# Kernel tuning notes

Hardware: AMD Instinct MI355X
Metric: run time of the kernel (lower is better)

The kernel has to match this reference:

```python
import jax, jax.numpy as jnp
import numpy as np

B, T, N_EMBED, HEADSIZE = 16, 2048, 1024, 128


def setup_inputs() -> dict:
    key = jax.random.key(0)
    kx, kq, kk, kv = jax.random.split(key, 4)
    x = jax.random.normal(kx, (B, T, N_EMBED), dtype=jnp.float32)
    # nn.Linear(n_embed, headsize, bias=False): y = x @ W, W stored [n_embed, headsize]
    s = (1.0 / np.sqrt(N_EMBED)).astype(np.float32)
    Wq = jax.random.normal(kq, (N_EMBED, HEADSIZE), dtype=jnp.float32) * s
    Wk = jax.random.normal(kk, (N_EMBED, HEADSIZE), dtype=jnp.float32) * s
    Wv = jax.random.normal(kv, (N_EMBED, HEADSIZE), dtype=jnp.float32) * s
    return {"x": x, "Wq": Wq, "Wk": Wk, "Wv": Wv}


def reference(x, Wq, Wk, Wv):
    Bsz, Tlen, C = x.shape
    q = x @ Wq  # [B, T, H]
    k = x @ Wk  # [B, T, H]
    v = x @ Wv  # [B, T, H]
    scale = C ** (-0.5)  # NOTE: original scales by n_embed**-0.5, not headsize**-0.5
    wt = jnp.einsum('bqh,bkh->bqk', q, k) * scale  # [B, T, T]
    causal = jnp.tril(jnp.ones((Tlen, Tlen), dtype=bool))
    wt = jnp.where(causal, wt, -jnp.inf)
    wt = jax.nn.softmax(wt, axis=-1)
    # dropout is identity in eval mode
    out = jnp.einsum('bqk,bkh->bqh', wt, v)  # [B, T, H]
    return out
```

## Files before the change

### kernel.cpp

```cpp
#include <hip/hip_runtime.h>
#include <hip/hip_bf16.h>

#define BATCH 16
#define TLEN 2048
#define CDIM 1024
#define HDIM 128

typedef __attribute__((ext_vector_type(8))) short bf16x8;
typedef __attribute__((ext_vector_type(4))) float f32x4;
typedef __attribute__((ext_vector_type(16))) float f32x16;
typedef __attribute__((ext_vector_type(4))) unsigned short u16x4;
typedef __attribute__((ext_vector_type(8))) unsigned short u16x8;

static __device__ __forceinline__ unsigned short f2bf(float f) {
    __hip_bfloat16 h = __float2bfloat16(f);
    return *(unsigned short*)&h;
}
static __device__ __forceinline__ unsigned pkbf(float a, float b) {
    return (unsigned)f2bf(a) | ((unsigned)f2bf(b) << 16);
}
static __device__ __forceinline__ int part_offs(int qc) {
    return qc + ((qc * qc - 2 * qc + (qc & 1)) >> 2);
}

typedef const __attribute__((address_space(1))) unsigned int* gas_t;
typedef __attribute__((address_space(3))) unsigned int* las_t;
static __device__ __forceinline__ void gl_lds16(const void* g, void* l) {
    __builtin_amdgcn_global_load_lds((gas_t)g, (las_t)l, 16, 0, 0);
}

__global__ __launch_bounds__(256) void pack_w(
    const float* __restrict__ Wq, const float* __restrict__ Wk,
    const float* __restrict__ Wv, unsigned short* __restrict__ wtb)
{
    const int which = blockIdx.y;
    const float* W = (which == 0) ? Wq : (which == 1) ? Wk : Wv;
    const int n = blockIdx.x >> 2;
    const int k = (blockIdx.x & 3) * 256 + threadIdx.x;
    wtb[((size_t)which * 128 + n) * 1024 + k] = f2bf(W[(size_t)k * 128 + n]);
}

__global__ __launch_bounds__(256, 2) void qkv_fused(
    const float* __restrict__ x, const unsigned short* __restrict__ wtb,
    unsigned short* __restrict__ qb, unsigned short* __restrict__ kb,
    unsigned short* __restrict__ vtb)
{
    __shared__ unsigned short Abf[2][64 * 32];
    __shared__ unsigned short Bs[2][384 * 32];

    const int tid  = threadIdx.x;
    const int lane = tid & 63, wid = tid >> 6;
    const int c = lane & 15, g = lane >> 4;
    const int m0 = blockIdx.x * 64;

    const int arow = tid >> 2;
    const int acol = (tid & 3) * 8;
    const float* xsrc = x + (size_t)(m0 + arow) * CDIM + acol;

    const int brow = lane >> 2, bcol = (lane & 3) * 8;

    f32x4 acc[4][6];
#pragma unroll
    for (int i = 0; i < 4; ++i)
#pragma unroll
        for (int j = 0; j < 6; ++j) acc[i][j] = (f32x4){0.f, 0.f, 0.f, 0.f};

    float4 a0, a1;

#define GLA(k0_)                                                             \
    { a0 = *(const float4*)(xsrc + (k0_));                                   \
      a1 = *(const float4*)(xsrc + (k0_) + 4); }

#define CVTW(bi_)                                                            \
    { u16x8 t_;                                                              \
      t_[0]=f2bf(a0.x); t_[1]=f2bf(a0.y); t_[2]=f2bf(a0.z); t_[3]=f2bf(a0.w);\
      t_[4]=f2bf(a1.x); t_[5]=f2bf(a1.y); t_[6]=f2bf(a1.z); t_[7]=f2bf(a1.w);\
      *(u16x8*)((char*)Abf[bi_] + arow * 64 + acol * 2) = t_; }

#define STB(k0_, bi_)                                                        \
    { _Pragma("unroll")                                                      \
      for (int i_ = 0; i_ < 6; ++i_) {                                       \
          const int seg_ = wid * 6 + i_;                                     \
          const unsigned short* src_ = wtb +                                 \
              (size_t)(seg_ * 16 + brow) * 1024 + (k0_) + bcol;              \
          gl_lds16(src_, (char*)Bs[bi_] + seg_ * 1024);                      \
      } }

    GLA(0);
    STB(0, 0);
    CVTW(0);
    __syncthreads();

#pragma unroll 1
    for (int kt = 0; kt < 32; ++kt) {
        const int bi = kt & 1;
        if (kt < 31) {
            GLA((kt + 1) * 32);
            STB((kt + 1) * 32, bi ^ 1);
        }

        bf16x8 af[4], bf[6];
#pragma unroll
        for (int mf = 0; mf < 4; ++mf)
            af[mf] = *(const bf16x8*)((char*)Abf[bi] + (mf * 16 + c) * 64 + g * 16);
#pragma unroll
        for (int nf = 0; nf < 6; ++nf)
            bf[nf] = *(const bf16x8*)((char*)Bs[bi] + (wid * 96 + nf * 16 + c) * 64 + g * 16);
#pragma unroll
        for (int mf = 0; mf < 4; ++mf)
#pragma unroll
            for (int nf = 0; nf < 6; ++nf)
                acc[mf][nf] = __builtin_amdgcn_mfma_f32_16x16x32_bf16(
                    af[mf], bf[nf], acc[mf][nf], 0, 0, 0);

        if (kt < 31) CVTW(bi ^ 1);
        __syncthreads();
    }

#pragma unroll
    for (int mf = 0; mf < 4; ++mf) {
#pragma unroll
        for (int nf = 0; nf < 6; ++nf) {
            const int col0 = wid * 96 + nf * 16;
            const int nt = col0 >> 7;
            const int nc = (col0 & 127) + c;
            const int m = m0 + mf * 16 + g * 4;
            if (nt == 0) {
#pragma unroll
                for (int r = 0; r < 4; ++r)
                    qb[(size_t)(m + r) * HDIM + nc] = f2bf(acc[mf][nf][r] * 0.03125f);
            } else if (nt == 1) {
#pragma unroll
                for (int r = 0; r < 4; ++r)
                    kb[(size_t)(m + r) * HDIM + nc] = f2bf(acc[mf][nf][r]);
            } else {
                const int b = m >> 11, tl = m & (TLEN - 1);
                u16x4 o;
                o[0] = f2bf(acc[mf][nf][0]); o[1] = f2bf(acc[mf][nf][1]);
                o[2] = f2bf(acc[mf][nf][2]); o[3] = f2bf(acc[mf][nf][3]);
                *(u16x4*)(vtb + ((size_t)b * HDIM + nc) * TLEN + tl) = o;
            }
        }
    }
#undef GLA
#undef CVTW
#undef STB
}

__global__ __launch_bounds__(256, 2) void attn_partial(
    const short* __restrict__ qb, const short* __restrict__ kb,
    const short* __restrict__ vtb,
    unsigned short* __restrict__ Opart, float* __restrict__ mpart,
    float* __restrict__ lpart)
{
    const int kc = blockIdx.x;
    const int qc = blockIdx.y;
    const int b  = blockIdx.z;
    if (kc > (qc >> 1)) return;
    const int kv_base = kc * 256;
    const int qrel = qc * 128 - kv_base;
    int NT = ((qrel + 127) >> 6) + 1; if (NT > 4) NT = 4;

    __shared__ unsigned short Ks[2][64 * 128];
    __shared__ unsigned short Vs[2][128 * 64];

    const int tid  = threadIdx.x;
    const int wid  = tid >> 6;
    const int lane = tid & 63;
    const int c5 = lane & 31, hi = lane >> 5;
    const int q0w = qc * 128 + wid * 32;
    const int qg  = q0w + c5;
    const int pidx = b * 72 + part_offs(qc) + kc;

    const short* Kb  = kb  + (size_t)b * TLEN * HDIM;
    const short* Vtb = vtb + (size_t)b * HDIM * TLEN;

    bf16x8 qf[8];
#pragma unroll
    for (int ks = 0; ks < 8; ++ks)
        qf[ks] = *(const bf16x8*)(qb + ((size_t)b * TLEN + qg) * HDIM + ks * 16 + hi * 8);

    bf16x8 kst[4], vst[4];

#define GLOAD(kv0_)                                                          \
    {                                                                        \
        _Pragma("unroll")                                                    \
        for (int it = 0; it < 4; ++it) {                                     \
            const int o = tid * 16 + it * 4096;                              \
            const int kr = o >> 8, kcb = o & 0xF0;                           \
            kst[it] = *(const bf16x8*)((const char*)Kb +                     \
                        (size_t)((kv0_) + kr) * 256 + kcb);                  \
            const int vr = o >> 7, vcb = o & 0x70;                           \
            vst[it] = *(const bf16x8*)((const char*)Vtb +                    \
                        (size_t)vr * (TLEN * 2) + (size_t)(kv0_) * 2 + vcb); \
        }                                                                    \
    }
#define SSTORE(bi_)                                                          \
    {                                                                        \
        _Pragma("unroll")                                                    \
        for (int it = 0; it < 4; ++it) {                                     \
            const int o = tid * 16 + it * 4096;                              \
            const int kr = o >> 8, kcb = o & 0xF0;                           \
            *(bf16x8*)((char*)Ks[bi_] + kr * 256 + (kcb ^ ((kr & 7) << 4))) = kst[it]; \
            const int vr = o >> 7, vcb = o & 0x70;                           \
            *(bf16x8*)((char*)Vs[bi_] + vr * 128 + (vcb ^ ((vr & 7) << 4))) = vst[it]; \
        }                                                                    \
    }

    GLOAD(kv_base);
    SSTORE(0);
    __syncthreads();

    f32x16 oacc[4];
#pragma unroll
    for (int i = 0; i < 4; ++i)
#pragma unroll
        for (int r = 0; r < 16; ++r) oacc[i][r] = 0.f;
    float m_r = -1e30f;
    float l_r = 0.f;

#pragma unroll 1
    for (int t = 0; t < NT; ++t) {
        const int bi = t & 1;
        if (t + 1 < NT) GLOAD(kv_base + 64 * (t + 1));

        const int kv0 = kv_base + 64 * t;
        if (kv0 <= q0w + 31) {
            f32x16 s0, s1;
#pragma unroll
            for (int r = 0; r < 16; ++r) { s0[r] = 0.f; s1[r] = 0.f; }
            __builtin_amdgcn_s_setprio(1);
#pragma unroll
            for (int ks = 0; ks < 8; ++ks) {
                const int col = ks * 32 + hi * 16;
                const int off0 = c5 * 256 + (col ^ ((c5 & 7) << 4));
                const int off1 = (32 + c5) * 256 + (col ^ ((c5 & 7) << 4));
                bf16x8 a0 = *(const bf16x8*)((char*)Ks[bi] + off0);
                bf16x8 a1 = *(const bf16x8*)((char*)Ks[bi] + off1);
                s0 = __builtin_amdgcn_mfma_f32_32x32x16_bf16(a0, qf[ks], s0, 0, 0, 0);
                s1 = __builtin_amdgcn_mfma_f32_32x32x16_bf16(a1, qf[ks], s1, 0, 0, 0);
            }
            __builtin_amdgcn_s_setprio(0);

            if (kv0 + 63 > q0w) {
#pragma unroll
                for (int r = 0; r < 16; ++r) {
                    const int key0 = kv0 + (r & 3) + 8 * (r >> 2) + 4 * hi;
                    if (key0 > qg)      s0[r] = -INFINITY;
                    if (key0 + 32 > qg) s1[r] = -INFINITY;
                }
            }

            float t8[8];
#pragma unroll
            for (int i = 0; i < 8; ++i)
                t8[i] = fmaxf(fmaxf(s0[2*i], s0[2*i+1]), fmaxf(s1[2*i], s1[2*i+1]));
            float smax = fmaxf(fmaxf(fmaxf(t8[0], t8[1]), fmaxf(t8[2], t8[3])),
                               fmaxf(fmaxf(t8[4], t8[5]), fmaxf(t8[6], t8[7])));
            smax = fmaxf(smax, __shfl_xor(smax, 32));

            const bool defer = __all(smax - m_r <= 8.0f);
            const float mnew = defer ? m_r : fmaxf(m_r, smax);
            if (!defer) {
                const float alpha = __expf(m_r - mnew);
                l_r *= alpha;
#pragma unroll
                for (int hb = 0; hb < 4; ++hb) oacc[hb] = oacc[hb] * alpha;
            }
            m_r = mnew;

#pragma unroll
            for (int r = 0; r < 16; ++r) {
                s0[r] = __expf(s0[r] - mnew);
                s1[r] = __expf(s1[r] - mnew);
            }
            float a8[8];
#pragma unroll
            for (int i = 0; i < 8; ++i)
                a8[i] = (s0[2*i] + s0[2*i+1]) + (s1[2*i] + s1[2*i+1]);
            float psum = ((a8[0] + a8[1]) + (a8[2] + a8[3])) +
                         ((a8[4] + a8[5]) + (a8[6] + a8[7]));
            psum += __shfl_xor(psum, 32);
            l_r += psum;

            bf16x8 pa[4];
#pragma unroll
            for (int kb2 = 0; kb2 < 2; ++kb2) {
#pragma unroll
                for (int par = 0; par < 2; ++par) {
                    const int e = par * 8;
                    float v0, v1, v2, v3, v4, v5, v6, v7;
                    if (kb2 == 0) {
                        v0=s0[e+0]; v1=s0[e+1]; v2=s0[e+2]; v3=s0[e+3];
                        v4=s0[e+4]; v5=s0[e+5]; v6=s0[e+6]; v7=s0[e+7];
                    } else {
                        v0=s1[e+0]; v1=s1[e+1]; v2=s1[e+2]; v3=s1[e+3];
                        v4=s1[e+4]; v5=s1[e+5]; v6=s1[e+6]; v7=s1[e+7];
                    }
                    const unsigned w0 = pkbf(v0, v1), w1 = pkbf(v2, v3);
                    const unsigned w2 = pkbf(v4, v5), w3 = pkbf(v6, v7);
                    const unsigned X0 = hi ? w0 : w2;
                    const unsigned X1 = hi ? w1 : w3;
                    const unsigned R0 = (unsigned)__shfl_xor((int)X0, 32);
                    const unsigned R1 = (unsigned)__shfl_xor((int)X1, 32);
                    union { unsigned w[4]; bf16x8 v; } uu;
                    uu.w[0] = hi ? R0 : w0;  uu.w[1] = hi ? R1 : w1;
                    uu.w[2] = hi ? w2 : R0;  uu.w[3] = hi ? w3 : R1;
                    pa[kb2 * 2 + par] = uu.v;
                }
            }

            __builtin_amdgcn_s_setprio(1);
#pragma unroll
            for (int hb = 0; hb < 4; ++hb) {
                const int row = hb * 32 + c5;
#pragma unroll
                for (int ks = 0; ks < 4; ++ks) {
                    const int off = row * 128 + ((ks * 32 + hi * 16) ^ ((row & 7) << 4));
                    bf16x8 va = *(const bf16x8*)((char*)Vs[bi] + off);
                    oacc[hb] = __builtin_amdgcn_mfma_f32_32x32x16_bf16(va, pa[ks], oacc[hb], 0, 0, 0);
                }
            }
            __builtin_amdgcn_s_setprio(0);
        }

        if (t + 1 < NT) {
            SSTORE(bi ^ 1);
            __syncthreads();
        }
    }

    __syncthreads();
    char* sl = (char*)Ks + wid * 8192;
#pragma unroll
    for (int hb = 0; hb < 4; ++hb)
#pragma unroll
        for (int rq = 0; rq < 4; ++rq) {
            u16x4 o4;
            o4[0] = f2bf(oacc[hb][rq * 4 + 0]);
            o4[1] = f2bf(oacc[hb][rq * 4 + 1]);
            o4[2] = f2bf(oacc[hb][rq * 4 + 2]);
            o4[3] = f2bf(oacc[hb][rq * 4 + 3]);
            const int off = c5 * 256 + ((hb * 64 + rq * 16 + hi * 8) ^ ((c5 & 7) << 4));
            *(u16x4*)(sl + off) = o4;
        }
    asm volatile("s_waitcnt lgkmcnt(0)" ::: "memory");
    __builtin_amdgcn_sched_barrier(0);

    const int qr = lane >> 1, hf = lane & 1;
    unsigned short* Og = Opart + (size_t)pidx * 128 * 128 +
                         (size_t)(wid * 32 + qr) * 128 + hf * 64;
#pragma unroll
    for (int i = 0; i < 8; ++i) {
        const int off = qr * 256 + ((hf * 128 + i * 16) ^ ((qr & 7) << 4));
        *(u16x8*)(Og + i * 8) = *(const u16x8*)(sl + off);
    }
    if (hi == 0) {
        mpart[(size_t)pidx * 128 + wid * 32 + c5] = m_r;
        lpart[(size_t)pidx * 128 + wid * 32 + c5] = l_r;
    }
#undef GLOAD
#undef SSTORE
}

__global__ __launch_bounds__(256) void attn_combine(
    const unsigned short* __restrict__ Opart, const float* __restrict__ mpart,
    const float* __restrict__ lpart, float* __restrict__ out)
{
    const int qc = blockIdx.x;
    const int b  = blockIdx.y;
    const int n  = (qc >> 1) + 1;
    const int base = b * 72 + part_offs(qc);
    const int t   = threadIdx.x;
    const int row = t >> 1;
    const int d0  = (t & 1) * 64;

    float M = -INFINITY;
    for (int p = 0; p < n; ++p)
        M = fmaxf(M, mpart[(size_t)(base + p) * 128 + row]);
    float L = 0.f;
    for (int p = 0; p < n; ++p)
        L += __expf(mpart[(size_t)(base + p) * 128 + row] - M) *
             lpart[(size_t)(base + p) * 128 + row];

    float acc[64];
#pragma unroll
    for (int i = 0; i < 64; ++i) acc[i] = 0.f;

    for (int p = 0; p < n; ++p) {
        const float w = __expf(mpart[(size_t)(base + p) * 128 + row] - M);
        const bf16x8* src = (const bf16x8*)(Opart +
            ((size_t)(base + p) * 128 + row) * 128 + d0);
#pragma unroll
        for (int j = 0; j < 8; ++j) {
            bf16x8 v = src[j];
#pragma unroll
            for (int e = 0; e < 8; ++e) {
                union { unsigned u; float f; } x;
                x.u = ((unsigned)(unsigned short)v[e]) << 16;
                acc[j * 8 + e] += w * x.f;
            }
        }
    }

    const float invL = 1.f / L;
    float4* dst = (float4*)(out + ((size_t)(b * TLEN + qc * 128 + row)) * 128 + d0);
#pragma unroll
    for (int i = 0; i < 16; ++i)
        dst[i] = make_float4(acc[4*i] * invL, acc[4*i+1] * invL,
                             acc[4*i+2] * invL, acc[4*i+3] * invL);
}

extern "C" void kernel_launch(void* const* d_in, const int* in_sizes, int n_in,
                              void* d_out, int out_size, void* d_ws, size_t ws_size,
                              hipStream_t stream)
{
    const float* x  = (const float*)d_in[0];
    const float* Wq = (const float*)d_in[1];
    const float* Wk = (const float*)d_in[2];
    const float* Wv = (const float*)d_in[3];
    float* outp = (float*)d_out;

    const size_t per = (size_t)BATCH * TLEN * HDIM;
    unsigned short* qb  = (unsigned short*)d_ws;
    unsigned short* kb  = qb + per;
    unsigned short* vtb = kb + per;
    unsigned short* wtb = vtb + per;
    unsigned short* Opart = wtb + 384 * 1024;
    float* mpart = (float*)(Opart + (size_t)1152 * 128 * 128);
    float* lpart = mpart + (size_t)1152 * 128;

    dim3 gw(512, 3);
    pack_w<<<gw, 256, 0, stream>>>(Wq, Wk, Wv, wtb);

    qkv_fused<<<512, 256, 0, stream>>>(x, wtb, qb, kb, vtb);

    dim3 g2(8, 16, BATCH);
    attn_partial<<<g2, 256, 0, stream>>>((const short*)qb, (const short*)kb,
                                         (const short*)vtb, Opart, mpart, lpart);

    dim3 g3(16, BATCH);
    attn_combine<<<g3, 256, 0, stream>>>(Opart, mpart, lpart, outp);
}
```

Before: 135.6 us.

## Stage fp32 x tiles via direct global-to-LDS loads with XOR swizzle

The QKV projection kernel now copies fp32 x tiles straight into LDS with gl_lds16 instead of going through registers and converting before the LDS store. The bf16 conversion moves to fragment-read time. Both the A and B LDS tiles gain XOR swizzles to avoid bank conflicts. This frees registers and makes the A load asynchronous, but it doubles A's LDS footprint and read traffic and repeats the conversions per wave (each wave converts the full A tile).

```diff
diff --git a/kernel.cpp b/kernel.cpp
--- a/kernel.cpp
+++ b/kernel.cpp
@@ -45,67 +45,65 @@
     unsigned short* __restrict__ qb, unsigned short* __restrict__ kb,
     unsigned short* __restrict__ vtb)
 {
-    __shared__ unsigned short Abf[2][64 * 32];
-    __shared__ unsigned short Bs[2][384 * 32];
+    __shared__ __align__(16) float          Axf[2][64 * 32];
+    __shared__ __align__(16) unsigned short Bs[2][384 * 32];
 
     const int tid  = threadIdx.x;
     const int lane = tid & 63, wid = tid >> 6;
     const int c = lane & 15, g = lane >> 4;
     const int m0 = blockIdx.x * 64;
 
-    const int arow = tid >> 2;
-    const int acol = (tid & 3) * 8;
-    const float* xsrc = x + (size_t)(m0 + arow) * CDIM + acol;
-
-    const int brow = lane >> 2, bcol = (lane & 3) * 8;
-
     f32x4 acc[4][6];
 #pragma unroll
     for (int i = 0; i < 4; ++i)
 #pragma unroll
         for (int j = 0; j < 6; ++j) acc[i][j] = (f32x4){0.f, 0.f, 0.f, 0.f};
 
-    float4 a0, a1;
-
-#define GLA(k0_)                                                             \
-    { a0 = *(const float4*)(xsrc + (k0_));                                   \
-      a1 = *(const float4*)(xsrc + (k0_) + 4); }
-
-#define CVTW(bi_)                                                            \
-    { u16x8 t_;                                                              \
-      t_[0]=f2bf(a0.x); t_[1]=f2bf(a0.y); t_[2]=f2bf(a0.z); t_[3]=f2bf(a0.w);\
-      t_[4]=f2bf(a1.x); t_[5]=f2bf(a1.y); t_[6]=f2bf(a1.z); t_[7]=f2bf(a1.w);\
-      *(u16x8*)((char*)Abf[bi_] + arow * 64 + acol * 2) = t_; }
-
-#define STB(k0_, bi_)                                                        \
+#define STAGE(k0_, bi_)                                                      \
     { _Pragma("unroll")                                                      \
+      for (int i_ = 0; i_ < 2; ++i_) {                                       \
+          const int seg_ = wid * 2 + i_;                                     \
+          const int row_ = seg_ * 8 + (lane >> 3);                           \
+          const int col_ = (((lane & 7) ^ (row_ & 7)) << 2);                 \
+          gl_lds16(x + (size_t)(m0 + row_) * CDIM + (k0_) + col_,            \
+                   (char*)Axf[bi_] + seg_ * 1024);                           \
+      }                                                                      \
+      _Pragma("unroll")                                                      \
       for (int i_ = 0; i_ < 6; ++i_) {                                       \
           const int seg_ = wid * 6 + i_;                                     \
-          const unsigned short* src_ = wtb +                                 \
-              (size_t)(seg_ * 16 + brow) * 1024 + (k0_) + bcol;              \
-          gl_lds16(src_, (char*)Bs[bi_] + seg_ * 1024);                      \
+          const int row_ = seg_ * 16 + (lane >> 2);                          \
+          const int col_ = (((lane & 3) ^ ((row_ >> 1) & 3)) << 3);          \
+          gl_lds16(wtb + (size_t)row_ * 1024 + (k0_) + col_,                 \
+                   (char*)Bs[bi_] + seg_ * 1024);                            \
       } }
 
-    GLA(0);
-    STB(0, 0);
-    CVTW(0);
+    STAGE(0, 0);
     __syncthreads();
 
 #pragma unroll 1
     for (int kt = 0; kt < 32; ++kt) {
         const int bi = kt & 1;
-        if (kt < 31) {
-            GLA((kt + 1) * 32);
-            STB((kt + 1) * 32, bi ^ 1);
-        }
+        if (kt < 31) STAGE((kt + 1) * 32, bi ^ 1);
 
         bf16x8 af[4], bf[6];
 #pragma unroll
-        for (int mf = 0; mf < 4; ++mf)
-            af[mf] = *(const bf16x8*)((char*)Abf[bi] + (mf * 16 + c) * 64 + g * 16);
-#pragma unroll
-        for (int nf = 0; nf < 6; ++nf)
-            bf[nf] = *(const bf16x8*)((char*)Bs[bi] + (wid * 96 + nf * 16 + c) * 64 + g * 16);
+        for (int mf = 0; mf < 4; ++mf) {
+            const int rm = mf * 16 + c;
+            const char* base = (const char*)Axf[bi] + rm * 128;
+            f32x4 lo = *(const f32x4*)(base + ((((2 * g)     ^ (rm & 7)) << 4)));
+            f32x4 hi = *(const f32x4*)(base + ((((2 * g + 1) ^ (rm & 7)) << 4)));
+            bf16x8 t;
+            t[0] = f2bf(lo[0]); t[1] = f2bf(lo[1]); t[2] = f2bf(lo[2]); t[3] = f2bf(lo[3]);
+            t[4] = f2bf(hi[0]); t[5] = f2bf(hi[1]); t[6] = f2bf(hi[2]); t[7] = f2bf(hi[3]);
+            af[mf] = t;
+        }
+#pragma unroll
+        for (int nf = 0; nf < 6; ++nf) {
+            const int rn = wid * 96 + nf * 16 + c;
+            bf[nf] = *(const bf16x8*)((const char*)Bs[bi] + rn * 64 +
+                                      ((g ^ ((rn >> 1) & 3)) << 4));
+        }
+
 #pragma unroll
         for (int mf = 0; mf < 4; ++mf)
 #pragma unroll
@@ -113,7 +111,6 @@
                 acc[mf][nf] = __builtin_amdgcn_mfma_f32_16x16x32_bf16(
                     af[mf], bf[nf], acc[mf][nf], 0, 0, 0);
 
-        if (kt < 31) CVTW(bi ^ 1);
         __syncthreads();
     }
 
@@ -142,9 +139,7 @@
             }
         }
     }
-#undef GLA
-#undef CVTW
-#undef STB
+#undef STAGE
 }
 
 __global__ __launch_bounds__(256, 2) void attn_partial(
```

After: 133.9 us. No clear change (-1.3%).
